# Optimization experiments

Hardware: AMD Instinct MI355X
Metric: run time of the kernel (lower is better)

Reference implementation:

```python
import jax, jax.numpy as jnp
import numpy as np

# Fixed Gauss-Legendre quadrature on [-A, A] replacing scipy.integrate.quadrature
A = 5.0
NQ = 64
_x, _w = np.polynomial.legendre.leggauss(NQ)
GL_X = jnp.asarray(_x * A, dtype=jnp.float32)  # nodes scaled to [-5, 5]
# Fold exp(-z^2/2)/sqrt(2*pi) and interval scaling into the weights
GL_W_EFF = jnp.asarray(_w * A * np.exp(-(_x * A) ** 2 / 2.0) / np.sqrt(2.0 * np.pi), dtype=jnp.float32)

# given_params=True constants
SIG_M1, SIG_M2, SIG_I = 1.0, 1.0, 1.0
SIG_M1N1, SIG_M2N2 = 1.0, 0.5
SIG_N1I, SIG_N2I = 0.5, 1.9
SIG_M1W, SIG_M2W = 2.8, -2.2
TAU, DT = 100.0, 20.0


def setup_inputs() -> dict:
    key = jax.random.key(0)
    B, T = 8192, 2048
    u = jax.random.normal(key, (B, T), dtype=jnp.float32)
    return {"u": u}


def reference(u):
    B, T = u.shape
    alpha = jnp.float32(DT / TAU)

    def step(carry, u_t):
        k1, k2, v = carry  # each [B]
        delta = jnp.sqrt(SIG_M1**2 * k1**2 + SIG_M2**2 * k2**2 + SIG_I**2 * u_t**2)  # [B]
        # gauss_int[b] = int_{-A}^{A} (1 - tanh(delta_b z)^2) exp(-z^2/2) dz / sqrt(2pi)
        dphi = 1.0 - jnp.tanh(delta[:, None] * GL_X[None, :]) ** 2  # [B, NQ]
        gauss_int = dphi @ GL_W_EFF  # [B]
        k1_new = k1 + (-k1 + SIG_M1N1 * gauss_int * k1 + SIG_N1I * gauss_int * v) * alpha
        k2_new = k2 + (-k2 + SIG_M2N2 * gauss_int * k2 + SIG_N2I * gauss_int * v) * alpha
        v_new = v + (-v + u_t) * alpha
        z = SIG_M1W * k1_new + SIG_M2W * k2_new
        return (k1_new, k2_new, v_new), z

    zeros = jnp.zeros((B,), dtype=u.dtype)
    _, z_seq = jax.lax.scan(step, (zeros, zeros, zeros), u.T)  # z_seq: [T, B]
    # z_hist: [B, T+1], column 0 is the zero initial state
    z_hist = jnp.concatenate([zeros[:, None], z_seq.T], axis=1)
    return z_hist
```

## Files before the change

### kernel.cpp

```cpp
#include <hip/hip_runtime.h>
#include <math.h>


#define Bsz   8192
#define Tlen  2048
#define TP1   2049
#define NQ    64
#define NG    2049
#define INV_H 32.0f
#define CHUNKS 16
#define CLEN  128
#define WARM  128
#define BLOCK 256
#define RPW   32
#define SROW  33
#define SIM_GRID (64 * CHUNKS)

#define WS_TAB 128

__device__ __forceinline__ void bar_nodrain() {
    asm volatile("s_waitcnt lgkmcnt(0)" ::: "memory");
    __builtin_amdgcn_s_barrier();
}
__device__ __forceinline__ void ds_fence() {
    asm volatile("s_waitcnt lgkmcnt(0)" ::: "memory");
}

__global__ __launch_bounds__(256) void setup_kernel(float* __restrict__ ws,
                                                    float* __restrict__ out) {
    __shared__ float  fx[NQ], fw[NQ];
    __shared__ double inv[NQ + 1];
    const int tid = threadIdx.x;
    if (tid <= NQ) inv[tid] = (tid == 0) ? 0.0 : 1.0 / (double)tid;
    __syncthreads();
    if (tid < NQ) {
        double z = cos(3.14159265358979323846 * (tid + 0.75) / (NQ + 0.5));
        double p1 = 1.0, p2 = 0.0, pp = 1.0;
        for (int it = 0; it < 4; ++it) {
            p1 = 1.0; p2 = 0.0;
            for (int j = 1; j <= NQ; ++j) {
                double p3 = p2; p2 = p1;
                p1 = ((2.0 * j - 1.0) * z * p2 - (j - 1.0) * p3) * inv[j];
            }
            pp = NQ * (z * p1 - p2) / (z * z - 1.0);
            if (it < 3) z -= p1 / pp;
        }
        double w  = 2.0 / ((1.0 - z * z) * pp * pp);
        double xs = z * 5.0;
        fx[tid] = (float)xs;
        fw[tid] = (float)(w * 5.0 * exp(-0.5 * xs * xs) * 0.3989422804014327);
    }
    __syncthreads();
    const int j = blockIdx.x * 256 + tid;
    if (j < NG) {
        const float d = sqrtf((float)j * (1.0f / INV_H));
        float acc = 0.0f;
        #pragma unroll 8
        for (int q = 0; q < NQ; ++q) {
            float t = tanhf(d * fx[q]);
            acc = fmaf(fw[q], 1.0f - t * t, acc);
        }
        ws[WS_TAB + j] = acc;
    }
    out[(size_t)j * TP1] = 0.0f;
}

__device__ __forceinline__ float step_one(float uu, float& k1, float& k2,
                                          float& v, const float* tab) {
    float s   = fmaf(k1, k1, fmaf(k2, k2, uu * uu));
    float idx = fminf(s * INV_H, 2046.999f);
    int   i0  = (int)idx;
    float f   = idx - (float)i0;
    float ga  = tab[i0];
    float gb  = tab[i0 + 1];
    float g   = fmaf(f, gb - ga, ga);
    float gv  = g * v;
    float nk1 = fmaf(k1, fmaf(0.2f, g, 0.8f), 0.10f * gv);
    float nk2 = fmaf(k2, fmaf(0.1f, g, 0.8f), 0.38f * gv);
    v  = fmaf(0.2f, uu - v, v);
    k1 = nk1; k2 = nk2;
    return fmaf(2.8f, nk1, -2.2f * nk2);
}

#define GLOAD(G, t) { _Pragma("unroll")                                       \
    for (int r = 0; r < 4; ++r)                                               \
        G[r] = *(const float4*)(up + (size_t)r * 8 * Tlen + (t)); }

#define STAGE(G) { asm volatile("" ::: "memory");  _Pragma("unroll")          \
    for (int r = 0; r < 4; ++r) {                                             \
        int b8 = (8 * r + srow) * SROW + scol;                                \
        sb[b8] = G[r].x; sb[b8+1] = G[r].y; sb[b8+2] = G[r].z;                \
        sb[b8+3] = G[r].w; }                                                  \
    ds_fence(); }

#define FLUSH(kw) { const int cb = t_out + 1 + 32 * (kw);                     \
    asm volatile("" ::: "memory");                                            \
    if (l < 32) { _Pragma("unroll") for (int j = 0; j < 32; ++j)              \
        sb[lbase + j] = zz[j]; }                                              \
    ds_fence();                                                               \
    _Pragma("unroll") for (int kk = 0; kk < 16; ++kk) {                       \
        int row = 2 * kk + (l >> 5);                                          \
        out[(size_t)(rowb + row) * TP1 + cb + (l & 31)] =                     \
            sb[row * SROW + (l & 31)];                                        \
    }                                                                         \
    ds_fence(); }

__global__ __launch_bounds__(BLOCK, 4) void sim_kernel(const float* __restrict__ u,
                                                       const float* __restrict__ ws,
                                                       float* __restrict__ out) {
    __shared__ float s_tabS[NG];
    __shared__ float s_st[4][RPW * SROW];
    const int tid = threadIdx.x;
    const int w   = tid >> 6;
    const int l   = tid & 63;
    float* sb = s_st[w];

    const int c    = blockIdx.x >> 6;
    const int rb   = blockIdx.x & 63;
    const int rowb = rb * 128 + w * RPW;
    const int t_out   = c * CLEN;
    const int t_begin = (t_out >= WARM) ? (t_out - WARM) : 0;

    const int srow = l >> 3;
    const int scol = (l & 7) * 4;
    const float* __restrict__ up = u + (size_t)(rowb + srow) * Tlen + scol;
    const int lbase = (l & 31) * SROW;

    float4 G[4];
    GLOAD(G, t_begin);

    {
        const float* g = ws + WS_TAB;
        float4 a0 = *(const float4*)(g + tid * 8);
        float4 a1 = *(const float4*)(g + tid * 8 + 4);
        *(float4*)&s_tabS[tid * 8]     = a0;
        *(float4*)&s_tabS[tid * 8 + 4] = a1;
        if (tid == 0) s_tabS[2048] = g[2048];
    }
    bar_nodrain();

    STAGE(G);
    GLOAD(G, t_begin + 32);

    float k1 = 0.f, k2 = 0.f, v = 0.f;

    for (int tb = t_begin; tb < t_out; tb += 32) {
        #pragma unroll
        for (int t2 = 0; t2 < 32; ++t2)
            step_one(sb[lbase + t2], k1, k2, v, s_tabS);
        ds_fence();
        STAGE(G);
        GLOAD(G, tb + 64);
    }

    float zz[32];
    #pragma unroll
    for (int kw = 0; kw < 4; ++kw) {
        #pragma unroll
        for (int t2 = 0; t2 < 32; ++t2)
            zz[t2] = step_one(sb[lbase + t2], k1, k2, v, s_tabS);
        ds_fence();
        FLUSH(kw);
        if (kw == 3) break;
        STAGE(G);
        int tn = t_out + 32 * kw + 64;
        if (tn > Tlen - 32) tn = Tlen - 32;
        GLOAD(G, tn);
    }
}

extern "C" void kernel_launch(void* const* d_in, const int* in_sizes, int n_in,
                              void* d_out, int out_size, void* d_ws, size_t ws_size,
                              hipStream_t stream) {
    const float* u = (const float*)d_in[0];
    float* out = (float*)d_out;
    float* ws  = (float*)d_ws;
    setup_kernel<<<32, 256, 0, stream>>>(ws, out);
    sim_kernel<<<SIM_GRID, BLOCK, 0, stream>>>(u, ws, out);
}
```

Before: 147.7 us.

## Pair table entries, lengthen chunks with shorter warmup, prefetch inputs into registers

The interpolation table is stored as float2 pairs, so each step does one LDS load instead of two. The time axis is split into fewer, longer chunks with a shorter warmup, which cuts the redundant warmup recurrence work. Each 32-step input tile is now read into registers before the next tile is staged, and the output flush is deferred so LDS traffic can overlap with the serial recurrence. In exchange, register use grows (launch bounds drop to 2 blocks per SM), there are fewer blocks, and the shorter warmup relies on the recurrence forgetting its state fast enough to stay accurate.

```diff
diff --git a/kernel.cpp b/kernel.cpp
--- a/kernel.cpp
+++ b/kernel.cpp
@@ -7,10 +7,11 @@
 #define TP1   2049
 #define NQ    64
 #define NG    2049
+#define NTAB2 2048
 #define INV_H 32.0f
-#define CHUNKS 16
-#define CLEN  128
-#define WARM  128
+#define CHUNKS 8
+#define CLEN  256
+#define WARM  96
 #define BLOCK 256
 #define RPW   32
 #define SROW  33
@@ -66,14 +67,13 @@
 }
 
 __device__ __forceinline__ float step_one(float uu, float& k1, float& k2,
-                                          float& v, const float* tab) {
+                                          float& v, const float2* s_tab) {
     float s   = fmaf(k1, k1, fmaf(k2, k2, uu * uu));
     float idx = fminf(s * INV_H, 2046.999f);
     int   i0  = (int)idx;
     float f   = idx - (float)i0;
-    float ga  = tab[i0];
-    float gb  = tab[i0 + 1];
-    float g   = fmaf(f, gb - ga, ga);
+    float2 g2 = s_tab[i0];
+    float g   = fmaf(f, g2.y - g2.x, g2.x);
     float gv  = g * v;
     float nk1 = fmaf(k1, fmaf(0.2f, g, 0.8f), 0.10f * gv);
     float nk2 = fmaf(k2, fmaf(0.1f, g, 0.8f), 0.38f * gv);
@@ -93,6 +93,10 @@
         sb[b8+3] = G[r].w; }                                                  \
     ds_fence(); }
 
+#define READBACK() { asm volatile("" ::: "memory"); _Pragma("unroll")         \
+    for (int j = 0; j < 32; ++j) U[j] = sb[lbase + j];                        \
+    ds_fence(); }
+
 #define FLUSH(kw) { const int cb = t_out + 1 + 32 * (kw);                     \
     asm volatile("" ::: "memory");                                            \
     if (l < 32) { _Pragma("unroll") for (int j = 0; j < 32; ++j)              \
@@ -105,11 +109,11 @@
     }                                                                         \
     ds_fence(); }
 
-__global__ __launch_bounds__(BLOCK, 4) void sim_kernel(const float* __restrict__ u,
+__global__ __launch_bounds__(BLOCK, 2) void sim_kernel(const float* __restrict__ u,
                                                        const float* __restrict__ ws,
                                                        float* __restrict__ out) {
-    __shared__ float s_tabS[NG];
-    __shared__ float s_st[4][RPW * SROW];
+    __shared__ float2 s_tab[NTAB2];
+    __shared__ float  s_st[4][RPW * SROW];
     const int tid = threadIdx.x;
     const int w   = tid >> 6;
     const int l   = tid & 63;
@@ -131,11 +135,16 @@
 
     {
         const float* g = ws + WS_TAB;
-        float4 a0 = *(const float4*)(g + tid * 8);
-        float4 a1 = *(const float4*)(g + tid * 8 + 4);
-        *(float4*)&s_tabS[tid * 8]     = a0;
-        *(float4*)&s_tabS[tid * 8 + 4] = a1;
-        if (tid == 0) s_tabS[2048] = g[2048];
+        #pragma unroll
+        for (int i = 0; i < NTAB2 / (BLOCK * 4); ++i) {
+            int k = (i * BLOCK + tid) * 4;
+            float4 a = *(const float4*)(g + k);
+            float  b = g[k + 4];
+            s_tab[k + 0] = make_float2(a.x, a.y);
+            s_tab[k + 1] = make_float2(a.y, a.z);
+            s_tab[k + 2] = make_float2(a.z, a.w);
+            s_tab[k + 3] = make_float2(a.w, b);
+        }
     }
     bar_nodrain();
 
@@ -143,30 +152,32 @@
     GLOAD(G, t_begin + 32);
 
     float k1 = 0.f, k2 = 0.f, v = 0.f;
+    float U[32];
 
     for (int tb = t_begin; tb < t_out; tb += 32) {
+        READBACK();
+        STAGE(G);
+        GLOAD(G, tb + 64);
         #pragma unroll
         for (int t2 = 0; t2 < 32; ++t2)
-            step_one(sb[lbase + t2], k1, k2, v, s_tabS);
-        ds_fence();
-        STAGE(G);
-        GLOAD(G, tb + 64);
+            step_one(U[t2], k1, k2, v, s_tab);
     }
 
     float zz[32];
     #pragma unroll
-    for (int kw = 0; kw < 4; ++kw) {
+    for (int kw = 0; kw < 8; ++kw) {
+        const int tb = t_out + 32 * kw;
+        READBACK();
+        if (kw > 0) FLUSH(kw - 1);
+        STAGE(G);
+        int tn = tb + 64;
+        if (tn > Tlen - 32) tn = Tlen - 32;
+        GLOAD(G, tn);
         #pragma unroll
         for (int t2 = 0; t2 < 32; ++t2)
-            zz[t2] = step_one(sb[lbase + t2], k1, k2, v, s_tabS);
-        ds_fence();
-        FLUSH(kw);
-        if (kw == 3) break;
-        STAGE(G);
-        int tn = t_out + 32 * kw + 64;
-        if (tn > Tlen - 32) tn = Tlen - 32;
-        GLOAD(G, tn);
+            zz[t2] = step_one(U[t2], k1, k2, v, s_tab);
     }
+    FLUSH(7);
 }
 
 extern "C" void kernel_launch(void* const* d_in, const int* in_sizes, int n_in,
```

After: 144.2 us. 2.3% less time.
